# Performance work log

Hardware: AMD Instinct MI355X
Metric: run time of the kernel (lower is better)

## Reference

```python
import jax, jax.numpy as jnp
import numpy as np

NUM_HEAD = 8  # matches init_kwargs num_head


def setup_inputs() -> dict:
    key = jax.random.key(0)
    ks = jax.random.split(key, 8)
    B, N, C, P = 2, 1024, 512, 256
    cluster_num = 8
    s = 0.02
    return {
        "x_token": jax.random.normal(ks[0], (B, N, C), jnp.float32),
        "x_path": jax.random.normal(ks[1], (B, N, P), jnp.float32),
        "idx_cluster": jax.random.randint(ks[2], (B, N), 0, cluster_num),
        "cluster_num": cluster_num,
        "Wq": jax.random.normal(ks[3], (C, C), jnp.float32) * s,
        "Wk": jax.random.normal(ks[4], (C, C), jnp.float32) * s,
        "Wv": jax.random.normal(ks[5], (C, C), jnp.float32) * s,
        "Wproj": jax.random.normal(ks[6], (C, C), jnp.float32) * s,
        "bproj": jnp.zeros((C,), jnp.float32),
    }


def reference(x_token, x_path, idx_cluster, cluster_num, Wq, Wk, Wv, Wproj, bproj):
    eps = 1e-6
    B, N, C = x_token.shape
    H = NUM_HEAD
    hd = C // H
    scale = hd ** -0.5

    # Linear projections (torch Linear: y = x @ W^T), qkv_bias=False
    q = x_token @ Wq.T
    k = x_token @ Wk.T
    v = (x_token @ Wv.T).reshape(B, N, H, hd).transpose(0, 2, 1, 3)  # (B,H,N,hd)

    qh = q.reshape(B, N, H, hd).transpose(0, 2, 1, 3)  # (B,H,N,hd)
    kh = k.reshape(B, N, H, hd).transpose(0, 2, 1, 3)

    # Raw scaled scores, computed once instead of per-cluster scatter/repeat
    s_ = jnp.einsum('bhid,bhjd->bhij', qh, kh) * scale  # (B,H,N,N)

    # One-hot cluster membership: (B, cluster_num, N)
    m = (idx_cluster[:, None, :] == jnp.arange(cluster_num)[None, :, None]).astype(s_.dtype)

    # attn_map[b,c,h,i,j] = s_[b,h,i,j] if idx[b,i]==c and idx[b,j]==c else 0
    attn_map = s_[:, None] * m[:, :, None, :, None] * m[:, :, None, None, :]  # (B,K,H,N,N)

    # Sum over clusters -> within-cluster scores, zeros elsewhere
    attn = attn_map.sum(axis=1)  # (B,H,N,N)

    # Custom eps-smoothed exp normalization (masked_fill on exact zeros, as in source)
    attn = jnp.where(attn == 0, jnp.float32(-1e9), attn).astype(jnp.float32)
    attn = jnp.exp(attn)
    attn = (attn + eps / N) / (attn.sum(axis=-1, keepdims=True) + eps)

    out = jnp.einsum('bhij,bhjd->bhid', attn, v)  # (B,H,N,hd)
    out = out.transpose(0, 2, 1, 3).reshape(B, N, C)
    out = out @ Wproj.T + bproj
    return out, attn_map
```

## Files before the change

kernel.cpp:

```cpp
#include <hip/hip_runtime.h>
#include <hip/hip_bf16.h>
#include <cstdint>
#include <cstddef>

#define NB   2
#define NN   1024
#define NC   512
#define NH   8
#define NHD  64
#define NK   8

typedef __attribute__((ext_vector_type(8))) short short8v;
typedef __attribute__((ext_vector_type(4))) short short4v;
typedef __attribute__((ext_vector_type(4))) float f32x4;

__device__ __forceinline__ short f2bf(float f) {
    union { float f; unsigned u; } v; v.f = f;
    unsigned r = v.u + 0x7FFFu + ((v.u >> 16) & 1u);
    return (short)(r >> 16);
}
__device__ __forceinline__ float bf2f(short s) {
    union { unsigned u; float f; } v;
    v.u = ((unsigned)(unsigned short)s) << 16;
    return v.f;
}

__global__ __launch_bounds__(256) void cast_kernel(
    const float* __restrict__ x, const float* __restrict__ wq,
    const float* __restrict__ wk, const float* __restrict__ wv,
    const float* __restrict__ wp,
    short* __restrict__ xb, short* __restrict__ wqb, short* __restrict__ wkb,
    short* __restrict__ wvb, short* __restrict__ wpb,
    float* __restrict__ rowsum) {
    int i = blockIdx.x * 256 + threadIdx.x;
    if (i < NB * NN * NC) xb[i] = f2bf(x[i]);
    if (i < NC * NC) {
        wqb[i] = f2bf(wq[i]);
        wkb[i] = f2bf(wk[i]);
        wvb[i] = f2bf(wv[i]);
        wpb[i] = f2bf(wp[i]);
    }
    if (i < NB * NH * NN) rowsum[i] = 0.f;
}

__global__ __launch_bounds__(256) void qkv_kernel(
    const short* __restrict__ xb, const short* __restrict__ wqb,
    const short* __restrict__ wkb, const short* __restrict__ wvb,
    short* __restrict__ qb, short* __restrict__ kb, short* __restrict__ vT) {
    __shared__ short As[64][40];
    __shared__ short Bs[64][40];
    const int tid = threadIdx.x;
    const int z = blockIdx.z;
    const short* Bsrc = (z == 0) ? wqb : ((z == 1) ? wkb : wvb);
    const int m0 = blockIdx.y * 64, n0 = blockIdx.x * 64;
    const int lane = tid & 63, wave = tid >> 6;
    const int wm = wave >> 1, wn = wave & 1, quad = lane >> 4, lr = lane & 15;
    const int row = tid >> 2, c0 = (tid & 3) * 8;
    f32x4 acc[2][2] = {};
    for (int kt = 0; kt < 512; kt += 32) {
        *(short8v*)&As[row][c0] = *(const short8v*)(xb + (m0 + row) * 512 + kt + c0);
        *(short8v*)&Bs[row][c0] = *(const short8v*)(Bsrc + (n0 + row) * 512 + kt + c0);
        __syncthreads();
        short8v a0 = *(short8v*)&As[wm * 32 + lr][quad * 8];
        short8v a1 = *(short8v*)&As[wm * 32 + 16 + lr][quad * 8];
        short8v b0 = *(short8v*)&Bs[wn * 32 + lr][quad * 8];
        short8v b1 = *(short8v*)&Bs[wn * 32 + 16 + lr][quad * 8];
        acc[0][0] = __builtin_amdgcn_mfma_f32_16x16x32_bf16(a0, b0, acc[0][0], 0, 0, 0);
        acc[0][1] = __builtin_amdgcn_mfma_f32_16x16x32_bf16(a0, b1, acc[0][1], 0, 0, 0);
        acc[1][0] = __builtin_amdgcn_mfma_f32_16x16x32_bf16(a1, b0, acc[1][0], 0, 0, 0);
        acc[1][1] = __builtin_amdgcn_mfma_f32_16x16x32_bf16(a1, b1, acc[1][1], 0, 0, 0);
        __syncthreads();
    }
    for (int sm = 0; sm < 2; sm++)
        for (int sn = 0; sn < 2; sn++)
            for (int r = 0; r < 4; r++) {
                int m = m0 + wm * 32 + sm * 16 + quad * 4 + r;
                int n = n0 + wn * 32 + sn * 16 + lr;
                short v = f2bf(acc[sm][sn][r]);
                if (z == 0) qb[m * 512 + n] = v;
                else if (z == 1) kb[m * 512 + n] = v;
                else {
                    int bb = m >> 10, i = m & 1023, h = n >> 6, d = n & 63;
                    vT[(size_t)(((bb * 8 + h) * 64 + d) << 10) + i] = v;
                }
            }
}

__global__ __launch_bounds__(256) void colsum_kernel(
    const short* __restrict__ vT, float* __restrict__ colsum) {
    __shared__ float cp[64][5];
    const int bh = blockIdx.x, t = threadIdx.x;
    const int d = t >> 2, seg = t & 3;
    const short* p = vT + (((size_t)(bh * 64 + d)) << 10) + seg * 256;
    float s = 0.f;
    for (int k = 0; k < 256; k += 8) {
        short8v v = *(const short8v*)(p + k);
        for (int j = 0; j < 8; j++) s += bf2f(v[j]);
    }
    cp[d][seg] = s;
    __syncthreads();
    if (t < 64) colsum[bh * 64 + t] = cp[t][0] + cp[t][1] + cp[t][2] + cp[t][3];
}

__global__ __launch_bounds__(256) void scores_attn_kernel(
    const short* __restrict__ qb, const short* __restrict__ kb,
    const int* __restrict__ idx, float* __restrict__ attn,
    short* __restrict__ eb, float* __restrict__ rowsum) {
    __shared__ short As[64][72];
    __shared__ short Bs[64][72];
    __shared__ float Ss[64][68];
    __shared__ int idxi[64], idxj[64];
    __shared__ float rowpart[64][17];
    const int tid = threadIdx.x;
    const int z = blockIdx.z;
    const int b = z >> 3, h = z & 7;
    const int i0 = blockIdx.y * 64, j0 = blockIdx.x * 64;
    const int lane = tid & 63, wave = tid >> 6;
    const int wm = wave >> 1, wn = wave & 1, quad = lane >> 4, lr = lane & 15;
    {
        int r0 = tid >> 3, cc = (tid & 7) * 8;
        *(short8v*)&As[r0][cc]      = *(const short8v*)(qb + (b * 1024 + i0 + r0) * 512 + h * 64 + cc);
        *(short8v*)&As[r0 + 32][cc] = *(const short8v*)(qb + (b * 1024 + i0 + r0 + 32) * 512 + h * 64 + cc);
        *(short8v*)&Bs[r0][cc]      = *(const short8v*)(kb + (b * 1024 + j0 + r0) * 512 + h * 64 + cc);
        *(short8v*)&Bs[r0 + 32][cc] = *(const short8v*)(kb + (b * 1024 + j0 + r0 + 32) * 512 + h * 64 + cc);
        if (tid < 64) idxi[tid] = idx[b * 1024 + i0 + tid];
        else if (tid < 128) idxj[tid - 64] = idx[b * 1024 + j0 + (tid - 64)];
    }
    __syncthreads();
    f32x4 acc[2][2] = {};
    for (int k0 = 0; k0 < 64; k0 += 32) {
        short8v a0 = *(short8v*)&As[wm * 32 + lr][k0 + quad * 8];
        short8v a1 = *(short8v*)&As[wm * 32 + 16 + lr][k0 + quad * 8];
        short8v b0 = *(short8v*)&Bs[wn * 32 + lr][k0 + quad * 8];
        short8v b1 = *(short8v*)&Bs[wn * 32 + 16 + lr][k0 + quad * 8];
        acc[0][0] = __builtin_amdgcn_mfma_f32_16x16x32_bf16(a0, b0, acc[0][0], 0, 0, 0);
        acc[0][1] = __builtin_amdgcn_mfma_f32_16x16x32_bf16(a0, b1, acc[0][1], 0, 0, 0);
        acc[1][0] = __builtin_amdgcn_mfma_f32_16x16x32_bf16(a1, b0, acc[1][0], 0, 0, 0);
        acc[1][1] = __builtin_amdgcn_mfma_f32_16x16x32_bf16(a1, b1, acc[1][1], 0, 0, 0);
    }
    for (int sm = 0; sm < 2; sm++)
        for (int sn = 0; sn < 2; sn++)
            for (int r = 0; r < 4; r++)
                Ss[wm * 32 + sm * 16 + quad * 4 + r][wn * 32 + sn * 16 + lr] = acc[sm][sn][r] * 0.125f;
    __syncthreads();
    const int rL = tid >> 4;
    const int cL = (tid & 15) * 4;
    const f32x4 zero4 = {0.f, 0.f, 0.f, 0.f};
    for (int ii = 0; ii < 4; ii++) {
        const int row = ii * 16 + rL;
        const int ci = idxi[row];
        f32x4 s4 = *(f32x4*)&Ss[row][cL];
        f32x4 m4;
        short4v e4;
        float rsum = 0.f;
        for (int kk = 0; kk < 4; kk++) {
            const bool in = (idxj[cL + kk] == ci);
            const float sv = s4[kk];
            m4[kk] = in ? sv : 0.f;
            const float ev = (in && sv != 0.f) ? __expf(sv) : 0.f;
            rsum += ev;
            e4[kk] = f2bf(ev);
        }
        rowpart[row][tid & 15] = rsum;
        float* base = attn + (((size_t)(b * 64 + h)) << 20) + (((size_t)(i0 + row)) << 10) + j0 + cL;
        for (int c = 0; c < 8; c++) {
            f32x4 w = (c == ci) ? m4 : zero4;
            __builtin_nontemporal_store(w, (f32x4*)(base + ((size_t)c << 23)));
        }
        *(short4v*)(eb + ((((size_t)z << 10) + i0 + row) << 10) + j0 + cL) = e4;
    }
    __syncthreads();
    if (tid < 64) {
        float v = 0.f;
        for (int s = 0; s < 16; s++) v += rowpart[tid][s];
        atomicAdd(&rowsum[(z << 10) + i0 + tid], v);
    }
}

__global__ __launch_bounds__(256) void pv_kernel(
    const short* __restrict__ eb, const short* __restrict__ vT,
    const float* __restrict__ rowsum, const float* __restrict__ colsum,
    short* __restrict__ oh) {
    __shared__ short As[64][40];
    __shared__ short Bs[64][40];
    __shared__ float invL[64], csL[64];
    const int tid = threadIdx.x;
    const int z = blockIdx.z;
    const int b = z >> 3, h = z & 7;
    const int i0 = blockIdx.y * 64;
    const int lane = tid & 63, wave = tid >> 6;
    const int wm = wave >> 1, wn = wave & 1, quad = lane >> 4, lr = lane & 15;
    const int row = tid >> 2, c0 = (tid & 3) * 8;
    if (tid < 64) invL[tid] = 1.f / (rowsum[(z << 10) + i0 + tid] + 1e-6f);
    else if (tid < 128) csL[tid - 64] = colsum[z * 64 + (tid - 64)];
    const short* Abase = eb + ((size_t)(z * 1024 + i0) << 10);
    const short* Bbase = vT + ((size_t)z << 16);
    f32x4 acc[2][2] = {};
    for (int kt = 0; kt < 1024; kt += 32) {
        *(short8v*)&As[row][c0] = *(const short8v*)(Abase + ((size_t)row << 10) + kt + c0);
        *(short8v*)&Bs[row][c0] = *(const short8v*)(Bbase + ((size_t)row << 10) + kt + c0);
        __syncthreads();
        short8v a0 = *(short8v*)&As[wm * 32 + lr][quad * 8];
        short8v a1 = *(short8v*)&As[wm * 32 + 16 + lr][quad * 8];
        short8v b0 = *(short8v*)&Bs[wn * 32 + lr][quad * 8];
        short8v b1 = *(short8v*)&Bs[wn * 32 + 16 + lr][quad * 8];
        acc[0][0] = __builtin_amdgcn_mfma_f32_16x16x32_bf16(a0, b0, acc[0][0], 0, 0, 0);
        acc[0][1] = __builtin_amdgcn_mfma_f32_16x16x32_bf16(a0, b1, acc[0][1], 0, 0, 0);
        acc[1][0] = __builtin_amdgcn_mfma_f32_16x16x32_bf16(a1, b0, acc[1][0], 0, 0, 0);
        acc[1][1] = __builtin_amdgcn_mfma_f32_16x16x32_bf16(a1, b1, acc[1][1], 0, 0, 0);
        __syncthreads();
    }
    const float epsN = 1e-6f / 1024.f;
    for (int sm = 0; sm < 2; sm++)
        for (int sn = 0; sn < 2; sn++)
            for (int r = 0; r < 4; r++) {
                int iLoc = wm * 32 + sm * 16 + quad * 4 + r;
                int d = wn * 32 + sn * 16 + lr;
                float val = (acc[sm][sn][r] + epsN * csL[d]) * invL[iLoc];
                oh[((size_t)(b * 1024 + i0 + iLoc)) * 512 + h * 64 + d] = f2bf(val);
            }
}

__global__ __launch_bounds__(256) void proj_kernel(
    const short* __restrict__ oh, const short* __restrict__ wpb,
    const float* __restrict__ bias, float* __restrict__ out) {
    __shared__ short As[64][40];
    __shared__ short Bs[64][40];
    const int tid = threadIdx.x;
    const int m0 = blockIdx.y * 64, n0 = blockIdx.x * 64;
    const int lane = tid & 63, wave = tid >> 6;
    const int wm = wave >> 1, wn = wave & 1, quad = lane >> 4, lr = lane & 15;
    const int row = tid >> 2, c0 = (tid & 3) * 8;
    f32x4 acc[2][2] = {};
    for (int kt = 0; kt < 512; kt += 32) {
        *(short8v*)&As[row][c0] = *(const short8v*)(oh + (m0 + row) * 512 + kt + c0);
        *(short8v*)&Bs[row][c0] = *(const short8v*)(wpb + (n0 + row) * 512 + kt + c0);
        __syncthreads();
        short8v a0 = *(short8v*)&As[wm * 32 + lr][quad * 8];
        short8v a1 = *(short8v*)&As[wm * 32 + 16 + lr][quad * 8];
        short8v b0 = *(short8v*)&Bs[wn * 32 + lr][quad * 8];
        short8v b1 = *(short8v*)&Bs[wn * 32 + 16 + lr][quad * 8];
        acc[0][0] = __builtin_amdgcn_mfma_f32_16x16x32_bf16(a0, b0, acc[0][0], 0, 0, 0);
        acc[0][1] = __builtin_amdgcn_mfma_f32_16x16x32_bf16(a0, b1, acc[0][1], 0, 0, 0);
        acc[1][0] = __builtin_amdgcn_mfma_f32_16x16x32_bf16(a1, b0, acc[1][0], 0, 0, 0);
        acc[1][1] = __builtin_amdgcn_mfma_f32_16x16x32_bf16(a1, b1, acc[1][1], 0, 0, 0);
        __syncthreads();
    }
    for (int sm = 0; sm < 2; sm++)
        for (int sn = 0; sn < 2; sn++)
            for (int r = 0; r < 4; r++) {
                int m = m0 + wm * 32 + sm * 16 + quad * 4 + r;
                int n = n0 + wn * 32 + sn * 16 + lr;
                out[(size_t)m * 512 + n] = acc[sm][sn][r] + bias[n];
            }
}

extern "C" void kernel_launch(void* const* d_in, const int* in_sizes, int n_in,
                              void* d_out, int out_size, void* d_ws, size_t ws_size,
                              hipStream_t stream) {
    const float* x     = (const float*)d_in[0];
    const int*   idx   = (const int*)d_in[2];
    const float* Wq    = (const float*)d_in[4];
    const float* Wk    = (const float*)d_in[5];
    const float* Wv    = (const float*)d_in[6];
    const float* Wp    = (const float*)d_in[7];
    const float* bproj = (const float*)d_in[8];

    float* out  = (float*)d_out;
    float* attn = out + (size_t)NB * NN * NC;

    char* ws = (char*)d_ws;
    short* xb  = (short*)(ws + 0);
    short* wqb = (short*)(ws + 2097152);
    short* wkb = (short*)(ws + 2621440);
    short* wvb = (short*)(ws + 3145728);
    short* wpb = (short*)(ws + 3670016);
    short* qb  = (short*)(ws + 4194304);
    short* kb  = (short*)(ws + 6291456);
    short* vT  = (short*)(ws + 8388608);
    short* oh  = (short*)(ws + 10485760);
    short* eb  = (short*)(ws + 12582912);
    float* rowsum = (float*)(ws + 46137344);
    float* colsum = (float*)(ws + 46202880);

    cast_kernel<<<4096, 256, 0, stream>>>(x, Wq, Wk, Wv, Wp, xb, wqb, wkb, wvb, wpb, rowsum);
    qkv_kernel<<<dim3(8, 32, 3), 256, 0, stream>>>(xb, wqb, wkb, wvb, qb, kb, vT);
    colsum_kernel<<<16, 256, 0, stream>>>(vT, colsum);
    scores_attn_kernel<<<dim3(16, 16, 16), 256, 0, stream>>>(qb, kb, idx, attn, eb, rowsum);
    pv_kernel<<<dim3(1, 16, 16), 256, 0, stream>>>(eb, vT, rowsum, colsum, oh);
    proj_kernel<<<dim3(8, 32, 1), 256, 0, stream>>>(oh, wpb, bproj, out);
}
```

Measured before the change: 607.3 us.

## Split attn_map zeroing into separate kernel and widen colsum/pv grids

A new kernel zero-fills the attn_map rows whose cluster does not match, skipping rows that scores_attn will write. scores_attn now stores one f32x4 per element to its own cluster slice instead of eight. This takes the zero-store traffic out of the scores kernel and lets it run ahead of the GEMM-heavy work. colsum and pv are also split over more blocks (pv uses 32-row tiles) to raise occupancy on the small grids, at the cost of less reuse of the V tile.

```diff
diff --git a/kernel.cpp b/kernel.cpp
--- a/kernel.cpp
+++ b/kernel.cpp
@@ -23,6 +23,23 @@
     union { unsigned u; float f; } v;
     v.u = ((unsigned)(unsigned short)s) << 16;
     return v.f;
+}
+
+__global__ __launch_bounds__(256) void zero_attn_kernel(
+    const int* __restrict__ idx, float* __restrict__ attn) {
+    __shared__ int rowskip[32];
+    const int blk = blockIdx.x;
+    const int itile = blk & 31, bch = blk >> 5;
+    const int c = (bch >> 3) & 7, b = bch >> 6;
+    const int t = threadIdx.x;
+    if (t < 32) rowskip[t] = (idx[b * 1024 + itile * 32 + t] == c);
+    __syncthreads();
+    float* base = attn + ((size_t)bch << 20) + ((size_t)itile << 15);
+    const f32x4 z = {0.f, 0.f, 0.f, 0.f};
+    for (int rr = 0; rr < 32; rr++) {
+        if (rowskip[rr]) continue;
+        __builtin_nontemporal_store(z, (f32x4*)(base + (rr << 10) + t * 4));
+    }
 }
 
 __global__ __launch_bounds__(256) void cast_kernel(
@@ -88,18 +105,24 @@
 
 __global__ __launch_bounds__(256) void colsum_kernel(
     const short* __restrict__ vT, float* __restrict__ colsum) {
-    __shared__ float cp[64][5];
-    const int bh = blockIdx.x, t = threadIdx.x;
-    const int d = t >> 2, seg = t & 3;
-    const short* p = vT + (((size_t)(bh * 64 + d)) << 10) + seg * 256;
+    __shared__ float cp[8][33];
+    const int blk = blockIdx.x;
+    const int bh = blk >> 3, dg = blk & 7;
+    const int t = threadIdx.x;
+    const int dl = t >> 5, seg = t & 31;
+    const short* p = vT + (((size_t)(bh * 64 + dg * 8 + dl)) << 10) + seg * 32;
     float s = 0.f;
-    for (int k = 0; k < 256; k += 8) {
+    for (int k = 0; k < 32; k += 8) {
         short8v v = *(const short8v*)(p + k);
         for (int j = 0; j < 8; j++) s += bf2f(v[j]);
     }
-    cp[d][seg] = s;
-    __syncthreads();
-    if (t < 64) colsum[bh * 64 + t] = cp[t][0] + cp[t][1] + cp[t][2] + cp[t][3];
+    cp[dl][seg] = s;
+    __syncthreads();
+    if (t < 8) {
+        float v = 0.f;
+        for (int s2 = 0; s2 < 32; s2++) v += cp[t][s2];
+        colsum[bh * 64 + dg * 8 + t] = v;
+    }
 }
 
 __global__ __launch_bounds__(256) void scores_attn_kernel(
@@ -145,7 +168,6 @@
     __syncthreads();
     const int rL = tid >> 4;
     const int cL = (tid & 15) * 4;
-    const f32x4 zero4 = {0.f, 0.f, 0.f, 0.f};
     for (int ii = 0; ii < 4; ii++) {
         const int row = ii * 16 + rL;
         const int ci = idxi[row];
@@ -162,11 +184,8 @@
             e4[kk] = f2bf(ev);
         }
         rowpart[row][tid & 15] = rsum;
-        float* base = attn + (((size_t)(b * 64 + h)) << 20) + (((size_t)(i0 + row)) << 10) + j0 + cL;
-        for (int c = 0; c < 8; c++) {
-            f32x4 w = (c == ci) ? m4 : zero4;
-            __builtin_nontemporal_store(w, (f32x4*)(base + ((size_t)c << 23)));
-        }
+        float* base = attn + (((size_t)(b * 64 + ci * 8 + h)) << 20) + (((size_t)(i0 + row)) << 10) + j0 + cL;
+        __builtin_nontemporal_store(m4, (f32x4*)base);
         *(short4v*)(eb + ((((size_t)z << 10) + i0 + row) << 10) + j0 + cL) = e4;
     }
     __syncthreads();
@@ -181,44 +200,41 @@
     const short* __restrict__ eb, const short* __restrict__ vT,
     const float* __restrict__ rowsum, const float* __restrict__ colsum,
     short* __restrict__ oh) {
-    __shared__ short As[64][40];
+    __shared__ short As[32][40];
     __shared__ short Bs[64][40];
-    __shared__ float invL[64], csL[64];
+    __shared__ float invL[32], csL[64];
     const int tid = threadIdx.x;
     const int z = blockIdx.z;
     const int b = z >> 3, h = z & 7;
-    const int i0 = blockIdx.y * 64;
+    const int i0 = blockIdx.y * 32;
     const int lane = tid & 63, wave = tid >> 6;
     const int wm = wave >> 1, wn = wave & 1, quad = lane >> 4, lr = lane & 15;
-    const int row = tid >> 2, c0 = (tid & 3) * 8;
-    if (tid < 64) invL[tid] = 1.f / (rowsum[(z << 10) + i0 + tid] + 1e-6f);
-    else if (tid < 128) csL[tid - 64] = colsum[z * 64 + (tid - 64)];
+    if (tid < 32) invL[tid] = 1.f / (rowsum[(z << 10) + i0 + tid] + 1e-6f);
+    else if (tid < 96) csL[tid - 32] = colsum[z * 64 + (tid - 32)];
     const short* Abase = eb + ((size_t)(z * 1024 + i0) << 10);
     const short* Bbase = vT + ((size_t)z << 16);
-    f32x4 acc[2][2] = {};
+    const int rowS = tid >> 2, c0 = (tid & 3) * 8;
+    f32x4 acc[2] = {};
     for (int kt = 0; kt < 1024; kt += 32) {
-        *(short8v*)&As[row][c0] = *(const short8v*)(Abase + ((size_t)row << 10) + kt + c0);
-        *(short8v*)&Bs[row][c0] = *(const short8v*)(Bbase + ((size_t)row << 10) + kt + c0);
-        __syncthreads();
-        short8v a0 = *(short8v*)&As[wm * 32 + lr][quad * 8];
-        short8v a1 = *(short8v*)&As[wm * 32 + 16 + lr][quad * 8];
+        if (tid < 128)
+            *(short8v*)&As[rowS][c0] = *(const short8v*)(Abase + ((size_t)rowS << 10) + kt + c0);
+        *(short8v*)&Bs[rowS & 63][c0] = *(const short8v*)(Bbase + ((size_t)(rowS & 63) << 10) + kt + c0);
+        __syncthreads();
+        short8v a0 = *(short8v*)&As[wm * 16 + lr][quad * 8];
         short8v b0 = *(short8v*)&Bs[wn * 32 + lr][quad * 8];
         short8v b1 = *(short8v*)&Bs[wn * 32 + 16 + lr][quad * 8];
-        acc[0][0] = __builtin_amdgcn_mfma_f32_16x16x32_bf16(a0, b0, acc[0][0], 0, 0, 0);
-        acc[0][1] = __builtin_amdgcn_mfma_f32_16x16x32_bf16(a0, b1, acc[0][1], 0, 0, 0);
-        acc[1][0] = __builtin_amdgcn_mfma_f32_16x16x32_bf16(a1, b0, acc[1][0], 0, 0, 0);
-        acc[1][1] = __builtin_amdgcn_mfma_f32_16x16x32_bf16(a1, b1, acc[1][1], 0, 0, 0);
+        acc[0] = __builtin_amdgcn_mfma_f32_16x16x32_bf16(a0, b0, acc[0], 0, 0, 0);
+        acc[1] = __builtin_amdgcn_mfma_f32_16x16x32_bf16(a0, b1, acc[1], 0, 0, 0);
         __syncthreads();
     }
     const float epsN = 1e-6f / 1024.f;
-    for (int sm = 0; sm < 2; sm++)
-        for (int sn = 0; sn < 2; sn++)
-            for (int r = 0; r < 4; r++) {
-                int iLoc = wm * 32 + sm * 16 + quad * 4 + r;
-                int d = wn * 32 + sn * 16 + lr;
-                float val = (acc[sm][sn][r] + epsN * csL[d]) * invL[iLoc];
-                oh[((size_t)(b * 1024 + i0 + iLoc)) * 512 + h * 64 + d] = f2bf(val);
-            }
+    for (int sn = 0; sn < 2; sn++)
+        for (int r = 0; r < 4; r++) {
+            int iLoc = wm * 16 + quad * 4 + r;
+            int d = wn * 32 + sn * 16 + lr;
+            float val = (acc[sn][r] + epsN * csL[d]) * invL[iLoc];
+            oh[((size_t)(b * 1024 + i0 + iLoc)) * 512 + h * 64 + d] = f2bf(val);
+        }
 }
 
 __global__ __launch_bounds__(256) void proj_kernel(
@@ -283,10 +299,11 @@
     float* rowsum = (float*)(ws + 46137344);
     float* colsum = (float*)(ws + 46202880);
 
+    zero_attn_kernel<<<4096, 256, 0, stream>>>(idx, attn);
     cast_kernel<<<4096, 256, 0, stream>>>(x, Wq, Wk, Wv, Wp, xb, wqb, wkb, wvb, wpb, rowsum);
     qkv_kernel<<<dim3(8, 32, 3), 256, 0, stream>>>(xb, wqb, wkb, wvb, qb, kb, vT);
-    colsum_kernel<<<16, 256, 0, stream>>>(vT, colsum);
+    colsum_kernel<<<128, 256, 0, stream>>>(vT, colsum);
     scores_attn_kernel<<<dim3(16, 16, 16), 256, 0, stream>>>(qb, kb, idx, attn, eb, rowsum);
-    pv_kernel<<<dim3(1, 16, 16), 256, 0, stream>>>(eb, vT, rowsum, colsum, oh);
+    pv_kernel<<<dim3(1, 32, 16), 256, 0, stream>>>(eb, vT, rowsum, colsum, oh);
     proj_kernel<<<dim3(8, 32, 1), 256, 0, stream>>>(oh, wpb, bproj, out);
 }
```

New measurement: 595.7 us. No clear change (-1.9%).

## Fuse score, softmax and PV into one attention kernel per query tile

Applied to the files above, without the earlier changes.

Merges the scores/attn-map kernel and the PV GEMM into one kernel. Each block owns a 64-row query tile and loops over all key tiles, keeping exp scores in shared memory and accumulating P·V in registers. This removes the bf16 exp-score intermediate in global memory (one write and one read) and the rowsum atomics and zeroing. The trade-off is a grid cut from 4096 blocks to 256 sequential-loop blocks, which may limit the parallelism available for the very large attn_map stores. The colsum kernel is also split across more blocks.

```diff
diff --git a/kernel.cpp b/kernel.cpp
--- a/kernel.cpp
+++ b/kernel.cpp
@@ -30,8 +30,7 @@
     const float* __restrict__ wk, const float* __restrict__ wv,
     const float* __restrict__ wp,
     short* __restrict__ xb, short* __restrict__ wqb, short* __restrict__ wkb,
-    short* __restrict__ wvb, short* __restrict__ wpb,
-    float* __restrict__ rowsum) {
+    short* __restrict__ wvb, short* __restrict__ wpb) {
     int i = blockIdx.x * 256 + threadIdx.x;
     if (i < NB * NN * NC) xb[i] = f2bf(x[i]);
     if (i < NC * NC) {
@@ -40,7 +39,6 @@
         wvb[i] = f2bf(wv[i]);
         wpb[i] = f2bf(wp[i]);
     }
-    if (i < NB * NH * NN) rowsum[i] = 0.f;
 }
 
 __global__ __launch_bounds__(256) void qkv_kernel(
@@ -88,135 +86,122 @@
 
 __global__ __launch_bounds__(256) void colsum_kernel(
     const short* __restrict__ vT, float* __restrict__ colsum) {
-    __shared__ float cp[64][5];
-    const int bh = blockIdx.x, t = threadIdx.x;
-    const int d = t >> 2, seg = t & 3;
-    const short* p = vT + (((size_t)(bh * 64 + d)) << 10) + seg * 256;
+    __shared__ float cp[8][33];
+    const int blk = blockIdx.x;
+    const int bh = blk >> 3, dg = blk & 7;
+    const int t = threadIdx.x;
+    const int dl = t >> 5, seg = t & 31;
+    const short* p = vT + (((size_t)(bh * 64 + dg * 8 + dl)) << 10) + seg * 32;
     float s = 0.f;
-    for (int k = 0; k < 256; k += 8) {
+    for (int k = 0; k < 32; k += 8) {
         short8v v = *(const short8v*)(p + k);
         for (int j = 0; j < 8; j++) s += bf2f(v[j]);
     }
-    cp[d][seg] = s;
+    cp[dl][seg] = s;
     __syncthreads();
-    if (t < 64) colsum[bh * 64 + t] = cp[t][0] + cp[t][1] + cp[t][2] + cp[t][3];
-}
-
-__global__ __launch_bounds__(256) void scores_attn_kernel(
+    if (t < 8) {
+        float v = 0.f;
+        for (int s2 = 0; s2 < 32; s2++) v += cp[t][s2];
+        colsum[bh * 64 + dg * 8 + t] = v;
+    }
+}
+
+__global__ __launch_bounds__(256) void attn_fused_kernel(
     const short* __restrict__ qb, const short* __restrict__ kb,
-    const int* __restrict__ idx, float* __restrict__ attn,
-    short* __restrict__ eb, float* __restrict__ rowsum) {
-    __shared__ short As[64][72];
-    __shared__ short Bs[64][72];
+    const short* __restrict__ vT, const int* __restrict__ idx,
+    const float* __restrict__ colsum, float* __restrict__ attn,
+    short* __restrict__ oh) {
+    __shared__ short Qs[64][72], Ks[64][72], Vs[64][72], Es[64][72];
     __shared__ float Ss[64][68];
     __shared__ int idxi[64], idxj[64];
     __shared__ float rowpart[64][17];
+    __shared__ float invL[64], csL[64];
     const int tid = threadIdx.x;
-    const int z = blockIdx.z;
-    const int b = z >> 3, h = z & 7;
-    const int i0 = blockIdx.y * 64, j0 = blockIdx.x * 64;
+    const int z = blockIdx.y, b = z >> 3, h = z & 7;
+    const int i0 = blockIdx.x * 64;
     const int lane = tid & 63, wave = tid >> 6;
     const int wm = wave >> 1, wn = wave & 1, quad = lane >> 4, lr = lane & 15;
-    {
-        int r0 = tid >> 3, cc = (tid & 7) * 8;
-        *(short8v*)&As[r0][cc]      = *(const short8v*)(qb + (b * 1024 + i0 + r0) * 512 + h * 64 + cc);
-        *(short8v*)&As[r0 + 32][cc] = *(const short8v*)(qb + (b * 1024 + i0 + r0 + 32) * 512 + h * 64 + cc);
-        *(short8v*)&Bs[r0][cc]      = *(const short8v*)(kb + (b * 1024 + j0 + r0) * 512 + h * 64 + cc);
-        *(short8v*)&Bs[r0 + 32][cc] = *(const short8v*)(kb + (b * 1024 + j0 + r0 + 32) * 512 + h * 64 + cc);
-        if (tid < 64) idxi[tid] = idx[b * 1024 + i0 + tid];
-        else if (tid < 128) idxj[tid - 64] = idx[b * 1024 + j0 + (tid - 64)];
-    }
-    __syncthreads();
-    f32x4 acc[2][2] = {};
-    for (int k0 = 0; k0 < 64; k0 += 32) {
-        short8v a0 = *(short8v*)&As[wm * 32 + lr][k0 + quad * 8];
-        short8v a1 = *(short8v*)&As[wm * 32 + 16 + lr][k0 + quad * 8];
-        short8v b0 = *(short8v*)&Bs[wn * 32 + lr][k0 + quad * 8];
-        short8v b1 = *(short8v*)&Bs[wn * 32 + 16 + lr][k0 + quad * 8];
-        acc[0][0] = __builtin_amdgcn_mfma_f32_16x16x32_bf16(a0, b0, acc[0][0], 0, 0, 0);
-        acc[0][1] = __builtin_amdgcn_mfma_f32_16x16x32_bf16(a0, b1, acc[0][1], 0, 0, 0);
-        acc[1][0] = __builtin_amdgcn_mfma_f32_16x16x32_bf16(a1, b0, acc[1][0], 0, 0, 0);
-        acc[1][1] = __builtin_amdgcn_mfma_f32_16x16x32_bf16(a1, b1, acc[1][1], 0, 0, 0);
-    }
-    for (int sm = 0; sm < 2; sm++)
-        for (int sn = 0; sn < 2; sn++)
-            for (int r = 0; r < 4; r++)
-                Ss[wm * 32 + sm * 16 + quad * 4 + r][wn * 32 + sn * 16 + lr] = acc[sm][sn][r] * 0.125f;
-    __syncthreads();
-    const int rL = tid >> 4;
-    const int cL = (tid & 15) * 4;
+    const int r0 = tid >> 3, cc = (tid & 7) * 8;
+    *(short8v*)&Qs[r0][cc]      = *(const short8v*)(qb + (b * 1024 + i0 + r0) * 512 + h * 64 + cc);
+    *(short8v*)&Qs[r0 + 32][cc] = *(const short8v*)(qb + (b * 1024 + i0 + r0 + 32) * 512 + h * 64 + cc);
+    if (tid < 64) { idxi[tid] = idx[b * 1024 + i0 + tid]; csL[tid] = colsum[z * 64 + tid]; }
+    f32x4 acc_o[2][2] = {};
+    float rsum[4] = {0.f, 0.f, 0.f, 0.f};
+    const int rL = tid >> 4, cI = tid & 15, cL = cI * 4;
     const f32x4 zero4 = {0.f, 0.f, 0.f, 0.f};
-    for (int ii = 0; ii < 4; ii++) {
-        const int row = ii * 16 + rL;
-        const int ci = idxi[row];
-        f32x4 s4 = *(f32x4*)&Ss[row][cL];
-        f32x4 m4;
-        short4v e4;
-        float rsum = 0.f;
-        for (int kk = 0; kk < 4; kk++) {
-            const bool in = (idxj[cL + kk] == ci);
-            const float sv = s4[kk];
-            m4[kk] = in ? sv : 0.f;
-            const float ev = (in && sv != 0.f) ? __expf(sv) : 0.f;
-            rsum += ev;
-            e4[kk] = f2bf(ev);
+    for (int jt = 0; jt < 16; jt++) {
+        const int j0 = jt * 64;
+        *(short8v*)&Ks[r0][cc]      = *(const short8v*)(kb + (b * 1024 + j0 + r0) * 512 + h * 64 + cc);
+        *(short8v*)&Ks[r0 + 32][cc] = *(const short8v*)(kb + (b * 1024 + j0 + r0 + 32) * 512 + h * 64 + cc);
+        *(short8v*)&Vs[r0][cc]      = *(const short8v*)(vT + ((size_t)z << 16) + (r0 << 10) + j0 + cc);
+        *(short8v*)&Vs[r0 + 32][cc] = *(const short8v*)(vT + ((size_t)z << 16) + ((r0 + 32) << 10) + j0 + cc);
+        if (tid < 64) idxj[tid] = idx[b * 1024 + j0 + tid];
+        __syncthreads();
+        f32x4 as[2][2] = {};
+        for (int k0 = 0; k0 < 64; k0 += 32) {
+            short8v a0 = *(short8v*)&Qs[wm * 32 + lr][k0 + quad * 8];
+            short8v a1 = *(short8v*)&Qs[wm * 32 + 16 + lr][k0 + quad * 8];
+            short8v b0 = *(short8v*)&Ks[wn * 32 + lr][k0 + quad * 8];
+            short8v b1 = *(short8v*)&Ks[wn * 32 + 16 + lr][k0 + quad * 8];
+            as[0][0] = __builtin_amdgcn_mfma_f32_16x16x32_bf16(a0, b0, as[0][0], 0, 0, 0);
+            as[0][1] = __builtin_amdgcn_mfma_f32_16x16x32_bf16(a0, b1, as[0][1], 0, 0, 0);
+            as[1][0] = __builtin_amdgcn_mfma_f32_16x16x32_bf16(a1, b0, as[1][0], 0, 0, 0);
+            as[1][1] = __builtin_amdgcn_mfma_f32_16x16x32_bf16(a1, b1, as[1][1], 0, 0, 0);
         }
-        rowpart[row][tid & 15] = rsum;
-        float* base = attn + (((size_t)(b * 64 + h)) << 20) + (((size_t)(i0 + row)) << 10) + j0 + cL;
-        for (int c = 0; c < 8; c++) {
-            f32x4 w = (c == ci) ? m4 : zero4;
-            __builtin_nontemporal_store(w, (f32x4*)(base + ((size_t)c << 23)));
+        for (int sm = 0; sm < 2; sm++)
+            for (int sn = 0; sn < 2; sn++)
+                for (int r = 0; r < 4; r++)
+                    Ss[wm * 32 + sm * 16 + quad * 4 + r][wn * 32 + sn * 16 + lr] = as[sm][sn][r] * 0.125f;
+        __syncthreads();
+        for (int ii = 0; ii < 4; ii++) {
+            const int row = ii * 16 + rL;
+            const int ci = idxi[row];
+            f32x4 s4 = *(f32x4*)&Ss[row][cL];
+            f32x4 m4;
+            short4v e4;
+            for (int kk = 0; kk < 4; kk++) {
+                const bool in = (idxj[cL + kk] == ci);
+                const float sv = s4[kk];
+                m4[kk] = in ? sv : 0.f;
+                const float ev = (in && sv != 0.f) ? __expf(sv) : 0.f;
+                rsum[ii] += ev;
+                e4[kk] = f2bf(ev);
+            }
+            float* base = attn + (((size_t)(b * 64 + h)) << 20) + (((size_t)(i0 + row)) << 10) + j0 + cL;
+            for (int c = 0; c < 8; c++) {
+                f32x4 w = (c == ci) ? m4 : zero4;
+                __builtin_nontemporal_store(w, (f32x4*)(base + ((size_t)c << 23)));
+            }
+            *(short4v*)&Es[row][cL] = e4;
         }
-        *(short4v*)(eb + ((((size_t)z << 10) + i0 + row) << 10) + j0 + cL) = e4;
-    }
+        __syncthreads();
+        for (int k0 = 0; k0 < 64; k0 += 32) {
+            short8v a0 = *(short8v*)&Es[wm * 32 + lr][k0 + quad * 8];
+            short8v a1 = *(short8v*)&Es[wm * 32 + 16 + lr][k0 + quad * 8];
+            short8v b0 = *(short8v*)&Vs[wn * 32 + lr][k0 + quad * 8];
+            short8v b1 = *(short8v*)&Vs[wn * 32 + 16 + lr][k0 + quad * 8];
+            acc_o[0][0] = __builtin_amdgcn_mfma_f32_16x16x32_bf16(a0, b0, acc_o[0][0], 0, 0, 0);
+            acc_o[0][1] = __builtin_amdgcn_mfma_f32_16x16x32_bf16(a0, b1, acc_o[0][1], 0, 0, 0);
+            acc_o[1][0] = __builtin_amdgcn_mfma_f32_16x16x32_bf16(a1, b0, acc_o[1][0], 0, 0, 0);
+            acc_o[1][1] = __builtin_amdgcn_mfma_f32_16x16x32_bf16(a1, b1, acc_o[1][1], 0, 0, 0);
+        }
+        __syncthreads();
+    }
+    for (int ii = 0; ii < 4; ii++) rowpart[ii * 16 + rL][cI] = rsum[ii];
     __syncthreads();
     if (tid < 64) {
         float v = 0.f;
         for (int s = 0; s < 16; s++) v += rowpart[tid][s];
-        atomicAdd(&rowsum[(z << 10) + i0 + tid], v);
-    }
-}
-
-__global__ __launch_bounds__(256) void pv_kernel(
-    const short* __restrict__ eb, const short* __restrict__ vT,
-    const float* __restrict__ rowsum, const float* __restrict__ colsum,
-    short* __restrict__ oh) {
-    __shared__ short As[64][40];
-    __shared__ short Bs[64][40];
-    __shared__ float invL[64], csL[64];
-    const int tid = threadIdx.x;
-    const int z = blockIdx.z;
-    const int b = z >> 3, h = z & 7;
-    const int i0 = blockIdx.y * 64;
-    const int lane = tid & 63, wave = tid >> 6;
-    const int wm = wave >> 1, wn = wave & 1, quad = lane >> 4, lr = lane & 15;
-    const int row = tid >> 2, c0 = (tid & 3) * 8;
-    if (tid < 64) invL[tid] = 1.f / (rowsum[(z << 10) + i0 + tid] + 1e-6f);
-    else if (tid < 128) csL[tid - 64] = colsum[z * 64 + (tid - 64)];
-    const short* Abase = eb + ((size_t)(z * 1024 + i0) << 10);
-    const short* Bbase = vT + ((size_t)z << 16);
-    f32x4 acc[2][2] = {};
-    for (int kt = 0; kt < 1024; kt += 32) {
-        *(short8v*)&As[row][c0] = *(const short8v*)(Abase + ((size_t)row << 10) + kt + c0);
-        *(short8v*)&Bs[row][c0] = *(const short8v*)(Bbase + ((size_t)row << 10) + kt + c0);
-        __syncthreads();
-        short8v a0 = *(short8v*)&As[wm * 32 + lr][quad * 8];
-        short8v a1 = *(short8v*)&As[wm * 32 + 16 + lr][quad * 8];
-        short8v b0 = *(short8v*)&Bs[wn * 32 + lr][quad * 8];
-        short8v b1 = *(short8v*)&Bs[wn * 32 + 16 + lr][quad * 8];
-        acc[0][0] = __builtin_amdgcn_mfma_f32_16x16x32_bf16(a0, b0, acc[0][0], 0, 0, 0);
-        acc[0][1] = __builtin_amdgcn_mfma_f32_16x16x32_bf16(a0, b1, acc[0][1], 0, 0, 0);
-        acc[1][0] = __builtin_amdgcn_mfma_f32_16x16x32_bf16(a1, b0, acc[1][0], 0, 0, 0);
-        acc[1][1] = __builtin_amdgcn_mfma_f32_16x16x32_bf16(a1, b1, acc[1][1], 0, 0, 0);
-        __syncthreads();
-    }
+        invL[tid] = 1.f / (v + 1e-6f);
+    }
+    __syncthreads();
     const float epsN = 1e-6f / 1024.f;
     for (int sm = 0; sm < 2; sm++)
         for (int sn = 0; sn < 2; sn++)
             for (int r = 0; r < 4; r++) {
                 int iLoc = wm * 32 + sm * 16 + quad * 4 + r;
                 int d = wn * 32 + sn * 16 + lr;
-                float val = (acc[sm][sn][r] + epsN * csL[d]) * invL[iLoc];
+                float val = (acc_o[sm][sn][r] + epsN * csL[d]) * invL[iLoc];
                 oh[((size_t)(b * 1024 + i0 + iLoc)) * 512 + h * 64 + d] = f2bf(val);
             }
 }
@@ -279,14 +264,11 @@
     short* kb  = (short*)(ws + 6291456);
     short* vT  = (short*)(ws + 8388608);
     short* oh  = (short*)(ws + 10485760);
-    short* eb  = (short*)(ws + 12582912);
-    float* rowsum = (float*)(ws + 46137344);
-    float* colsum = (float*)(ws + 46202880);
-
-    cast_kernel<<<4096, 256, 0, stream>>>(x, Wq, Wk, Wv, Wp, xb, wqb, wkb, wvb, wpb, rowsum);
+    float* colsum = (float*)(ws + 12582912);
+
+    cast_kernel<<<4096, 256, 0, stream>>>(x, Wq, Wk, Wv, Wp, xb, wqb, wkb, wvb, wpb);
     qkv_kernel<<<dim3(8, 32, 3), 256, 0, stream>>>(xb, wqb, wkb, wvb, qb, kb, vT);
-    colsum_kernel<<<16, 256, 0, stream>>>(vT, colsum);
-    scores_attn_kernel<<<dim3(16, 16, 16), 256, 0, stream>>>(qb, kb, idx, attn, eb, rowsum);
-    pv_kernel<<<dim3(1, 16, 16), 256, 0, stream>>>(eb, vT, rowsum, colsum, oh);
+    colsum_kernel<<<128, 256, 0, stream>>>(vT, colsum);
+    attn_fused_kernel<<<dim3(16, 16), 256, 0, stream>>>(qb, kb, vT, idx, colsum, attn, oh);
     proj_kernel<<<dim3(8, 32, 1), 256, 0, stream>>>(oh, wpb, bproj, out);
 }
```

After: 614.2 us. No clear change (+1.1%).
